# Optimization experiments

Hardware: AMD Instinct MI355X
Metric: run time of the kernel (lower is better)

The kernel has to match this reference:

```python
import jax, jax.numpy as jnp
import numpy as np

DS = 8  # avg-pool / upsample factor

def _avg_pool(x, ds):
    B, C, H, W = x.shape
    return x.reshape(B, C, H // ds, ds, W // ds, ds).mean(axis=(3, 5))

def _conv1x1(x, W, b):
    # 1x1 conv == per-pixel channel matmul
    return jnp.einsum('bchw,oc->bohw', x, W) + b[None, :, None, None]

def setup_inputs() -> dict:
    key = jax.random.key(0)
    ks = jax.random.split(key, 8)
    B, C, H, W = 8, 64, 256, 256
    scale = 1.0 / np.sqrt(C)
    return {
        'x':    jax.random.normal(ks[0], (B, C, H, W), dtype=jnp.float32),
        'diff': jax.random.normal(ks[1], (B, C, H, W), dtype=jnp.float32),
        'Wq': jax.random.normal(ks[2], (C, C), dtype=jnp.float32) * scale,
        'bq': jax.random.normal(ks[3], (C,), dtype=jnp.float32) * 0.01,
        'Wk': jax.random.normal(ks[4], (C, C), dtype=jnp.float32) * scale,
        'bk': jax.random.normal(ks[5], (C,), dtype=jnp.float32) * 0.01,
        'Wv': jax.random.normal(ks[6], (C, C), dtype=jnp.float32) * scale,
        'bv': jax.random.normal(ks[7], (C,), dtype=jnp.float32) * 0.01,
    }

def reference(x, diff, Wq, bq, Wk, bk, Wv, bv):
    C = x.shape[1]
    d = _avg_pool(diff, DS)                 # [B,C,h,w]
    B, _, h, w = d.shape
    N = h * w
    q = _conv1x1(d, Wq, bq).reshape(B, C, N)
    k = _conv1x1(d, Wk, bk).reshape(B, C, N)
    # energy[b,n,m] = sum_c q[b,c,n] * k[b,c,m], scaled by C^-0.5
    energy = jnp.einsum('bcn,bcm->bnm', q, k) * (C ** -0.5)
    attn = jax.nn.softmax(energy, axis=-1)  # [B,N,N]
    v = _conv1x1(_avg_pool(x, DS), Wv, bv).reshape(B, C, N)
    # out = v @ attn^T  (torch: bmm(value, attention.permute(0,2,1)))
    out = jnp.einsum('bcm,bnm->bcn', v, attn).reshape(B, C, h, w)
    # F.interpolate nearest with exact integer factor == pixel repeat
    out = jnp.repeat(jnp.repeat(out, DS, axis=2), DS, axis=3)
    return out + x
```

## Files before the change

kernel.cpp:

```cpp
#include <hip/hip_runtime.h>

#define BB 8
#define CC 64
#define HH 256
#define WW 256
#define DSF 8
#define HP 32
#define WP 32
#define NN 1024

typedef _Float16 f16x4 __attribute__((ext_vector_type(4)));
typedef float f32x4 __attribute__((ext_vector_type(4)));

__global__ __launch_bounds__(256) void k_pool(const float* __restrict__ x,
                                              const float* __restrict__ diff,
                                              float* __restrict__ dpool,
                                              float* __restrict__ pxpool) {
    int bid = blockIdx.x;
    int which = bid < 2048 ? 1 : 0;
    int r = bid & 2047;
    int plane = r >> 2;
    int g = r & 3;
    int t = threadIdx.x;
    int p = g * 256 + t;
    int prow = p >> 5, pcol = p & 31;
    const float* rb = (which ? x : diff)
                      + (size_t)plane * (HH * WW) + (size_t)(prow * 8) * WW + pcol * 8;
    f32x4 v[16];
#pragma unroll
    for (int rr = 0; rr < 8; ++rr) {
#pragma unroll
        for (int h = 0; h < 2; ++h)
            v[rr * 2 + h] = *(const f32x4*)(rb + rr * WW + 4 * h);
    }
    float s = 0.f;
#pragma unroll
    for (int i = 0; i < 16; ++i)
        s += (v[i][0] + v[i][1]) + (v[i][2] + v[i][3]);
    float* dst = (which ? pxpool : dpool) + (size_t)plane * NN + p;
    *dst = s * (1.f / 64.f);
}

__global__ __launch_bounds__(256) void k_proj(const float* __restrict__ dpool,
                                              const float* __restrict__ pxpool,
                                              const float* __restrict__ Wq, const float* __restrict__ bq,
                                              const float* __restrict__ Wk, const float* __restrict__ bk,
                                              const float* __restrict__ Wv, const float* __restrict__ bv,
                                              _Float16* __restrict__ qt, _Float16* __restrict__ kt,
                                              _Float16* __restrict__ vct) {
    __shared__ float Ws[64 * 65];
    __shared__ float dsh[64 * 68];
    int bid = blockIdx.x;
    int proj = bid >> 7;
    int rem = bid & 127;
    int b = rem >> 4;
    int n0 = (rem & 15) * 64;
    const float* Wm; const float* bias; const float* src;
    if (proj == 0)      { Wm = Wq; bias = bq; src = dpool; }
    else if (proj == 1) { Wm = Wk; bias = bk; src = dpool; }
    else                { Wm = Wv; bias = bv; src = pxpool; }
    int t = threadIdx.x;
#pragma unroll
    for (int i = 0; i < 16; ++i) {
        int e = t + i * 256;
        int o = e >> 6, c = e & 63;
        Ws[o * 65 + c] = Wm[e];
        dsh[o * 68 + c] = src[(size_t)(b * CC + o) * NN + n0 + c];
    }
    __syncthreads();
    int o = t & 63;
    int ng = t >> 6;
    float bb = bias[o];
    float4 acc[4];
#pragma unroll
    for (int j = 0; j < 4; ++j) acc[j] = make_float4(bb, bb, bb, bb);
#pragma unroll 8
    for (int c = 0; c < 64; ++c) {
        float wv = Ws[o * 65 + c];
        const float4* dr = (const float4*)(dsh + c * 68 + ng * 16);
#pragma unroll
        for (int j = 0; j < 4; ++j) {
            float4 d4 = dr[j];
            acc[j].x += wv * d4.x; acc[j].y += wv * d4.y;
            acc[j].z += wv * d4.z; acc[j].w += wv * d4.w;
        }
    }
    if (proj == 2) {
        _Float16* outp = vct + (size_t)(b * CC + o) * NN + n0 + ng * 16;
#pragma unroll
        for (int j = 0; j < 4; ++j) {
            f16x4 h;
            h[0] = (_Float16)acc[j].x; h[1] = (_Float16)acc[j].y;
            h[2] = (_Float16)acc[j].z; h[3] = (_Float16)acc[j].w;
            *(f16x4*)(outp + 4 * j) = h;
        }
    } else {
        __syncthreads();
#pragma unroll
        for (int j = 0; j < 4; ++j)
            *(float4*)(&dsh[o * 68 + ng * 16 + 4 * j]) = acc[j];
        __syncthreads();
        int nl = t & 63, og = t >> 6;
        float scale = (proj == 0) ? 0.125f : 1.0f;
        _Float16* outp = (proj == 0 ? qt : kt) + (size_t)(b * NN + n0 + nl) * CC + og * 16;
#pragma unroll
        for (int jj = 0; jj < 4; ++jj) {
            f16x4 h;
#pragma unroll
            for (int q4 = 0; q4 < 4; ++q4)
                h[q4] = (_Float16)(dsh[(og * 16 + 4 * jj + q4) * 68 + nl] * scale);
            *(f16x4*)(outp + 4 * jj) = h;
        }
    }
}

__global__ __launch_bounds__(256) void k_attn(const _Float16* __restrict__ qt,
                                              const _Float16* __restrict__ kt,
                                              const _Float16* __restrict__ vct,
                                              float* __restrict__ op) {
#define PS 1036
    __shared__ __align__(16) _Float16 P[16 * PS];
    __shared__ float part[4 * 16 * 65];
    __shared__ float wmax[4][16];
    __shared__ float wsum[4][16];
    int bid = blockIdx.x;
    int b = bid >> 6;
    int n0 = (bid & 63) * 16;
    int t = threadIdx.x;
    int w = t >> 6, l = t & 63;
    int lo = l & 15, g = l >> 4;

    const _Float16* qb = qt + (size_t)(b * NN + n0) * CC;
    const _Float16* kb = kt + (size_t)b * NN * CC;
    const _Float16* vb = vct + (size_t)b * CC * NN;

    f16x4 aq[4];
#pragma unroll
    for (int kc = 0; kc < 4; ++kc)
        aq[kc] = *(const f16x4*)(qb + lo * CC + 16 * kc + 4 * g);

    int mbase = w * 256;
    f32x4 e[16];
#pragma unroll
    for (int tm = 0; tm < 16; ++tm) e[tm] = (f32x4){0.f, 0.f, 0.f, 0.f};
#pragma unroll
    for (int tm = 0; tm < 16; ++tm) {
        int m = mbase + 16 * tm + lo;
        const _Float16* kr = kb + (size_t)m * CC + 4 * g;
#pragma unroll
        for (int kc = 0; kc < 4; ++kc) {
            f16x4 bk = *(const f16x4*)(kr + 16 * kc);
            e[tm] = __builtin_amdgcn_mfma_f32_16x16x16f16(aq[kc], bk, e[tm], 0, 0, 0);
        }
    }
    float mx[4], sm[4];
#pragma unroll
    for (int r = 0; r < 4; ++r) {
        float m_ = -1e30f;
#pragma unroll
        for (int tm = 0; tm < 16; ++tm) m_ = fmaxf(m_, e[tm][r]);
#pragma unroll
        for (int off = 8; off; off >>= 1) m_ = fmaxf(m_, __shfl_xor(m_, off));
        mx[r] = m_;
    }
    if (lo == 0) {
#pragma unroll
        for (int r = 0; r < 4; ++r) wmax[w][4 * g + r] = mx[r];
    }
    __syncthreads();
#pragma unroll
    for (int r = 0; r < 4; ++r) {
        int n = 4 * g + r;
        mx[r] = fmaxf(fmaxf(wmax[0][n], wmax[1][n]), fmaxf(wmax[2][n], wmax[3][n]));
        sm[r] = 0.f;
    }
#pragma unroll
    for (int tm = 0; tm < 16; ++tm) {
        int mcol = mbase + 16 * tm + lo;
#pragma unroll
        for (int r = 0; r < 4; ++r) {
            float p = __expf(e[tm][r] - mx[r]);
            sm[r] += p;
            P[(4 * g + r) * PS + mcol] = (_Float16)p;
        }
    }
#pragma unroll
    for (int r = 0; r < 4; ++r) {
#pragma unroll
        for (int off = 8; off; off >>= 1) sm[r] += __shfl_xor(sm[r], off);
    }
    if (lo == 0) {
#pragma unroll
        for (int r = 0; r < 4; ++r) wsum[w][4 * g + r] = sm[r];
    }
    f32x4 o4[4];
#pragma unroll
    for (int tc = 0; tc < 4; ++tc) o4[tc] = (f32x4){0.f, 0.f, 0.f, 0.f};
#pragma unroll
    for (int mk = 0; mk < 16; ++mk) {
        f16x4 pa = *(const f16x4*)(&P[lo * PS + mbase + 16 * mk + 4 * g]);
        const _Float16* vr = vb + mbase + 16 * mk + 4 * g;
#pragma unroll
        for (int tc = 0; tc < 4; ++tc) {
            f16x4 bv_ = *(const f16x4*)(vr + (size_t)(lo + 16 * tc) * NN);
            o4[tc] = __builtin_amdgcn_mfma_f32_16x16x16f16(pa, bv_, o4[tc], 0, 0, 0);
        }
    }
#pragma unroll
    for (int tc = 0; tc < 4; ++tc)
#pragma unroll
        for (int r = 0; r < 4; ++r)
            part[(w * 16 + 4 * g + r) * 65 + lo + 16 * tc] = o4[tc][r];
    __syncthreads();
#pragma unroll
    for (int i = 0; i < 4; ++i) {
        int e2 = t + i * 256;
        int c = e2 >> 4, n = e2 & 15;
        float s = part[(0 * 16 + n) * 65 + c] + part[(1 * 16 + n) * 65 + c] +
                  part[(2 * 16 + n) * 65 + c] + part[(3 * 16 + n) * 65 + c];
        float denom = wsum[0][n] + wsum[1][n] + wsum[2][n] + wsum[3][n];
        op[(size_t)(b * CC + c) * NN + n0 + n] = s / denom;
    }
#undef PS
}

__global__ __launch_bounds__(256) void k_out(const float* __restrict__ x,
                                             const float* __restrict__ op,
                                             float* __restrict__ out) {
    int t = threadIdx.x;
#pragma unroll
    for (int i = 0; i < 2; ++i) {
        size_t idx4 = (size_t)blockIdx.x * 512 + i * 256 + t;
        size_t flat = idx4 * 4;
        int w = (int)(flat & 255);
        int h = (int)((flat >> 8) & 255);
        int bc = (int)(flat >> 16);
        float ov = op[(size_t)bc * NN + (h >> 3) * WP + (w >> 3)];
        float4 xv = *(const float4*)(x + flat);
        f32x4 r = {xv.x + ov, xv.y + ov, xv.z + ov, xv.w + ov};
        __builtin_nontemporal_store(r, (f32x4*)(out + flat));
    }
}

extern "C" void kernel_launch(void* const* d_in, const int* in_sizes, int n_in,
                              void* d_out, int out_size, void* d_ws, size_t ws_size,
                              hipStream_t stream) {
    const float* x    = (const float*)d_in[0];
    const float* diff = (const float*)d_in[1];
    const float* Wq   = (const float*)d_in[2];
    const float* bq   = (const float*)d_in[3];
    const float* Wk   = (const float*)d_in[4];
    const float* bk   = (const float*)d_in[5];
    const float* Wv   = (const float*)d_in[6];
    const float* bv   = (const float*)d_in[7];
    float* ws = (float*)d_ws;
    float* dpool  = ws;
    float* pxpool = ws + 524288;
    float* op     = ws + 1048576;
    _Float16* qt  = (_Float16*)(ws + 1572864);
    _Float16* kt  = (_Float16*)(ws + 1835008);
    _Float16* vct = (_Float16*)(ws + 2097152);
    float* out = (float*)d_out;

    hipLaunchKernelGGL(k_pool, dim3(4096), dim3(256), 0, stream, x, diff, dpool, pxpool);
    hipLaunchKernelGGL(k_proj, dim3(384), dim3(256), 0, stream, dpool, pxpool,
                       Wq, bq, Wk, bk, Wv, bv, qt, kt, vct);
    hipLaunchKernelGGL(k_attn, dim3(512), dim3(256), 0, stream, qt, kt, vct, op);
    hipLaunchKernelGGL(k_out, dim3(16384), dim3(256), 0, stream, x, op, out);
}
```

Measured before the change: 122.8 us.

## Rewrite pooling kernel with async global-to-LDS double-buffered row loads

The pooling kernel now assigns one whole channel plane per block. Each wave streams 8-row strips with global_load_lds directly into double-buffered shared memory and uses manual vmcnt waits to overlap the next strip's load with reduction of the current one. Each wave load is fully coalesced across full rows, replacing per-thread strided 8x8 patch loads. Partial sums are combined with a cross-lane shuffle. The grid shrinks from 4096 to 1024 blocks, which relies on hand-counted waitcnt values that must exactly match the number of outstanding loads.

```diff
diff --git a/kernel.cpp b/kernel.cpp
--- a/kernel.cpp
+++ b/kernel.cpp
@@ -12,33 +12,54 @@
 typedef _Float16 f16x4 __attribute__((ext_vector_type(4)));
 typedef float f32x4 __attribute__((ext_vector_type(4)));
 
+__device__ __forceinline__ void gl_lds16(const float* g, float* l) {
+    __builtin_amdgcn_global_load_lds(
+        (const __attribute__((address_space(1))) unsigned int*)g,
+        (__attribute__((address_space(3))) unsigned int*)l, 16, 0, 0);
+}
+
 __global__ __launch_bounds__(256) void k_pool(const float* __restrict__ x,
                                               const float* __restrict__ diff,
                                               float* __restrict__ dpool,
                                               float* __restrict__ pxpool) {
+    __shared__ float buf[4][2][2048];
     int bid = blockIdx.x;
-    int which = bid < 2048 ? 1 : 0;
-    int r = bid & 2047;
-    int plane = r >> 2;
-    int g = r & 3;
-    int t = threadIdx.x;
-    int p = g * 256 + t;
-    int prow = p >> 5, pcol = p & 31;
-    const float* rb = (which ? x : diff)
-                      + (size_t)plane * (HH * WW) + (size_t)(prow * 8) * WW + pcol * 8;
-    f32x4 v[16];
-#pragma unroll
-    for (int rr = 0; rr < 8; ++rr) {
-#pragma unroll
-        for (int h = 0; h < 2; ++h)
-            v[rr * 2 + h] = *(const f32x4*)(rb + rr * WW + 4 * h);
-    }
-    float s = 0.f;
-#pragma unroll
-    for (int i = 0; i < 16; ++i)
-        s += (v[i][0] + v[i][1]) + (v[i][2] + v[i][3]);
-    float* dst = (which ? pxpool : dpool) + (size_t)plane * NN + p;
-    *dst = s * (1.f / 64.f);
+    int which = bid & 1;
+    int plane = bid >> 1;
+    const float* base = (which ? x : diff) + (size_t)plane * (HH * WW);
+    float* dst = (which ? pxpool : dpool) + (size_t)plane * NN;
+    int t = threadIdx.x;
+    int w = t >> 6, lane = t & 63;
+
+    auto stage = [&](int pr, int slot) {
+        const float* grow = base + (size_t)(pr * 8) * WW + lane * 4;
+#pragma unroll
+        for (int r = 0; r < 8; ++r)
+            gl_lds16(grow + r * WW, &buf[w][slot][r * 256]);
+    };
+
+    stage(w, 0);
+#pragma unroll
+    for (int it = 0; it < 8; ++it) {
+        int pr = 4 * it + w;
+        if (it < 7) stage(4 * (it + 1) + w, (it + 1) & 1);
+        if (it == 0)      asm volatile("s_waitcnt vmcnt(8)" ::: "memory");
+        else if (it < 7)  asm volatile("s_waitcnt vmcnt(9)" ::: "memory");
+        else              asm volatile("s_waitcnt vmcnt(1)" ::: "memory");
+        __builtin_amdgcn_sched_barrier(0);
+        int h = lane >> 5, pcol = lane & 31;
+        const f32x4* b4 = (const f32x4*)&buf[w][it & 1][0];
+        float s = 0.f;
+#pragma unroll
+        for (int rr = 0; rr < 4; ++rr) {
+            f32x4 a = b4[(h * 4 + rr) * 64 + pcol * 2];
+            f32x4 c = b4[(h * 4 + rr) * 64 + pcol * 2 + 1];
+            s += (a[0] + a[1]) + (a[2] + a[3]) + (c[0] + c[1]) + (c[2] + c[3]);
+        }
+        s += __shfl_xor(s, 32);
+        if (h == 0)
+            dst[pr * 32 + pcol] = s * (1.f / 64.f);
+    }
 }
 
 __global__ __launch_bounds__(256) void k_proj(const float* __restrict__ dpool,
@@ -262,7 +283,7 @@
     _Float16* vct = (_Float16*)(ws + 2097152);
     float* out = (float*)d_out;
 
-    hipLaunchKernelGGL(k_pool, dim3(4096), dim3(256), 0, stream, x, diff, dpool, pxpool);
+    hipLaunchKernelGGL(k_pool, dim3(1024), dim3(256), 0, stream, x, diff, dpool, pxpool);
     hipLaunchKernelGGL(k_proj, dim3(384), dim3(256), 0, stream, dpool, pxpool,
                        Wq, bq, Wk, bk, Wv, bv, qt, kt, vct);
     hipLaunchKernelGGL(k_attn, dim3(512), dim3(256), 0, stream, qt, kt, vct, op);
```

New measurement: 121.3 us. No clear change (-1.2%).
